# Optimization experiments

Hardware: AMD Instinct MI355X
Metric: run time of the kernel (lower is better)

The kernel has to match this reference:

```python
import jax, jax.numpy as jnp
import numpy as np

B, N, E, L, S = 8, 64, 256, 128, 2  # graphs, nodes, edges, latent dim, MPN steps


def setup_inputs() -> dict:
    key = jax.random.key(0)
    ks = jax.random.split(key, 16)

    def lin(k, fi, fo):
        return (jax.random.normal(k, (fi, fo), jnp.float32) / np.sqrt(fi).astype(np.float32))

    return {
        "x": jax.random.normal(ks[0], (B, N, L), jnp.float32),
        "edge_attr": jax.random.normal(ks[1], (B, E, L), jnp.float32),
        "u": jax.random.normal(ks[2], (B, L), jnp.float32),
        "spdist": jax.random.uniform(ks[3], (B, N, N), jnp.float32),
        "edge_index": jax.random.randint(ks[4], (B, 2, E), 0, N),
        # encoders
        "W_node_enc": lin(ks[5], 2 * L + 1, L), "b_node_enc": jnp.zeros(L, jnp.float32),
        "W_edge_enc": lin(ks[6], L, L), "b_edge_enc": jnp.zeros(L, jnp.float32),
        "W_glob_enc": lin(ks[7], L, L), "b_glob_enc": jnp.zeros(L, jnp.float32),
        # per-step edge / node update MLPs (stacked over S steps)
        "W_edge_upd": jnp.stack([lin(ks[8 + s], 4 * L, L) for s in range(S)]),
        "b_edge_upd": jnp.zeros((S, L), jnp.float32),
        "W_node_upd": jnp.stack([lin(ks[10 + s], 3 * L, L) for s in range(S)]),
        "b_node_upd": jnp.zeros((S, L), jnp.float32),
        # final edge scorer (per_dest_embedding_to_score)
        "W_score": lin(ks[12], L, 1), "b_score": jnp.zeros(1, jnp.float32),
    }


def reference(x, edge_attr, u, spdist, edge_index,
              W_node_enc, b_node_enc, W_edge_enc, b_edge_enc,
              W_glob_enc, b_glob_enc, W_edge_upd, b_edge_upd,
              W_node_upd, b_node_upd, W_score, b_score):
    act = jax.nn.leaky_relu  # torch LeakyReLU default slope 0.01
    n_steps = W_edge_upd.shape[0]

    def per_graph(xg, eg, ug, sdg, eig):
        Ng, Lg = xg.shape
        Eg = eg.shape[0]
        src, dst = eig[0], eig[1]
        # Augmented node features: graph copy d, node i -> [x_i, x_d, spdist[d, i]]
        # (matches x.repeat(N,1) / x.repeat_interleave(N,0) + chunk(N))
        x_tile = jnp.broadcast_to(xg[None, :, :], (Ng, Ng, Lg))
        x_dest = jnp.broadcast_to(xg[:, None, :], (Ng, Ng, Lg))
        xa = jnp.concatenate([x_tile, x_dest, sdg[..., None]], axis=-1)  # [Nd, N, 2L+1]
        h = act(xa @ W_node_enc + b_node_enc)                            # [Nd, N, L]
        ee = act(eg @ W_edge_enc + b_edge_enc)                           # [E, L]
        ee = jnp.broadcast_to(ee[None], (Ng, Eg, Lg))                    # [Nd, E, L]
        gg = act(ug @ W_glob_enc + b_glob_enc)                           # [L]
        for s in range(n_steps):
            gb_e = jnp.broadcast_to(gg, (Ng, Eg, Lg))
            ein = jnp.concatenate([ee, h[:, src], h[:, dst], gb_e], axis=-1)  # [Nd, E, 4L]
            ee = ee + act(ein @ W_edge_upd[s] + b_edge_upd[s])
            agg = jax.vmap(lambda ef: jax.ops.segment_sum(ef, dst, num_segments=Ng))(ee)  # [Nd, N, L]
            gb_n = jnp.broadcast_to(gg, (Ng, Ng, Lg))
            nin = jnp.concatenate([h, agg, gb_n], axis=-1)                    # [Nd, N, 3L]
            h = h + act(nin @ W_node_upd[s] + b_node_upd[s])
        scores = (ee @ W_score + b_score)[..., 0]  # [Nd, E]
        # reshape(N, -1).t().flatten() per graph -> [E * N]
        return scores.T.reshape(-1)

    out = jax.vmap(per_graph)(x, edge_attr, u, spdist, edge_index)  # [B, E*N]
    return out.reshape(-1)
```

## Files before the change

### kernel.cpp

```cpp
#include <hip/hip_runtime.h>
#include <hip/hip_bf16.h>


typedef __attribute__((ext_vector_type(8))) __bf16 bf16x8;
typedef __attribute__((ext_vector_type(4))) __bf16 bf16x4;
typedef __attribute__((ext_vector_type(4))) float  floatx4;

#define MFMA16(a, b, c) __builtin_amdgcn_mfma_f32_16x16x32_bf16((a), (b), (c), 0, 0, 0)

__device__ __forceinline__ float leaky(float x) { return x > 0.f ? x : 0.01f * x; }

#define WS_WT     0
#define WS_XAP    327680
#define WS_XDP    589824
#define WS_EE0    851968
#define WS_CE     1376256
#define WS_CN     1384448
#define WS_CSROFF 1392640
#define WS_CSREID 1394944

#define LDE 140

__global__ __launch_bounds__(256) void mpn_prep(
    const float* __restrict__ x,
    const float* __restrict__ ea,
    const float* __restrict__ u,
    const int*   __restrict__ eidx,
    const float* __restrict__ Wne,
    const float* __restrict__ bne,
    const float* __restrict__ Wee,
    const float* __restrict__ bee,
    const float* __restrict__ Wge,
    const float* __restrict__ bge,
    const float* __restrict__ Weu,
    const float* __restrict__ beu,
    const float* __restrict__ Wnu,
    const float* __restrict__ bnu,
    char* __restrict__ ws)
{
  __shared__ __align__(16) __bf16 smem[384 * LDE];

  const int b = blockIdx.x, tid = threadIdx.x;
  __bf16* wt  = (__bf16*)(ws + WS_WT);
  float*  xap = (float*)(ws + WS_XAP);
  float*  xdp = (float*)(ws + WS_XDP);
  __bf16* ee0 = (__bf16*)(ws + WS_EE0);
  float*  cev = (float*)(ws + WS_CE);
  float*  cnv = (float*)(ws + WS_CN);
  int* csroff = (int*)(ws + WS_CSROFF);
  int* csreid = (int*)(ws + WS_CSREID);

  if (b < 20) {
    const int m = b >> 1, half = b & 1;
    const int s = m / 5, t = m % 5;
    const float* src = (t < 3) ? (Weu + (size_t)(s*512 + t*128)*128)
                               : (Wnu + (size_t)(s*384 + (t-3)*128)*128);
    for (int it = 0; it < 4; ++it) {
      int p = it*256 + tid;
      int mq = half*4 + (p >> 8);
      int c  = (p >> 6) & 3;
      int l  = p & 63;
      int fr = mq*16 + (l & 15);
      int kb = c*32 + (l >> 4)*8;
      __bf16* dst = &wt[m*16384 + ((mq*4 + c)*64 + l)*8];
      #pragma unroll
      for (int j = 0; j < 8; ++j)
        dst[j] = (__bf16)src[(kb + j)*128 + fr];
    }
  } else if (b < 28) {
    const int g = b - 20;
    __shared__ float gg_sh[128];
    __shared__ int dst_sh[256];
    __shared__ int cnt_sh[64];
    __shared__ int off_sh[65];
    if (tid < 128) {
      float acc = bge[tid];
      for (int k = 0; k < 128; ++k)
        acc += u[g*128 + k] * Wge[k*128 + tid];
      gg_sh[tid] = leaky(acc);
    }
    dst_sh[tid] = eidx[g*512 + 256 + tid];
    __syncthreads();
    {
      const int s = tid >> 7, f = tid & 127;
      float ac = beu[s*128 + f];
      float an = bnu[s*128 + f];
      #pragma unroll 8
      for (int k = 0; k < 128; ++k) {
        float gk = gg_sh[k];
        ac += gk * Weu[(s*512 + 384 + k)*128 + f];
        an += gk * Wnu[(s*384 + 256 + k)*128 + f];
      }
      cev[(g*2 + s)*128 + f] = ac;
      cnv[(g*2 + s)*128 + f] = an;
    }
    if (tid < 64) {
      int c = 0;
      for (int e = 0; e < 256; ++e) c += (dst_sh[e] == tid) ? 1 : 0;
      cnt_sh[tid] = c;
    }
    __syncthreads();
    if (tid == 0) {
      int o = 0;
      for (int n = 0; n < 64; ++n) { off_sh[n] = o; o += cnt_sh[n]; }
      off_sh[64] = o;
    }
    __syncthreads();
    if (tid < 65) csroff[g*72 + tid] = off_sh[tid];
    if (tid < 64) {
      int o = off_sh[tid];
      for (int e = 0; e < 256; ++e)
        if (dst_sh[e] == tid) csreid[g*256 + (o++)] = e;
    }
  } else if (b < 36) {
    const int g = b - 28;
    __bf16* s_a = smem;
    __bf16* s_w = smem + 256*LDE;
    #pragma unroll
    for (int it = 0; it < 32; ++it) {
      int c = it*256 + tid;
      int row = c >> 5, f4 = (c & 31)*4;
      floatx4 v = *(const floatx4*)&ea[(size_t)(g*256 + row)*128 + f4];
      bf16x4 o;
      #pragma unroll
      for (int r = 0; r < 4; ++r) o[r] = (__bf16)v[r];
      *(bf16x4*)&s_a[row*LDE + f4] = o;
    }
    #pragma unroll 8
    for (int it = 0; it < 64; ++it) {
      int k = it*2 + (tid >> 7), f = tid & 127;
      s_w[f*LDE + k] = (__bf16)Wee[k*128 + f];
    }
    __syncthreads();
    const int w = tid >> 6, l = tid & 63, q = l >> 4, xn = l & 15;
    bf16x8 bea[4][4];
    #pragma unroll
    for (int t = 0; t < 4; ++t) {
      int e = w*64 + t*16 + xn;
      #pragma unroll
      for (int c = 0; c < 4; ++c)
        bea[t][c] = *(const bf16x8*)&s_a[e*LDE + c*32 + q*8];
    }
    #pragma unroll
    for (int m = 0; m < 8; ++m) {
      floatx4 acc[4];
      #pragma unroll
      for (int t = 0; t < 4; ++t) acc[t] = (floatx4)0.f;
      const int fr = m*16 + xn;
      #pragma unroll
      for (int c = 0; c < 4; ++c) {
        bf16x8 aw = *(const bf16x8*)&s_w[fr*LDE + c*32 + q*8];
        #pragma unroll
        for (int t = 0; t < 4; ++t) acc[t] = MFMA16(aw, bea[t][c], acc[t]);
      }
      const int f0 = m*16 + q*4;
      floatx4 b4 = *(const floatx4*)&bee[f0];
      #pragma unroll
      for (int t = 0; t < 4; ++t) {
        int e = w*64 + t*16 + xn;
        bf16x4 o;
        #pragma unroll
        for (int r = 0; r < 4; ++r) o[r] = (__bf16)leaky(acc[t][r] + b4[r]);
        *(bf16x4*)&ee0[(size_t)(g*256 + e)*128 + f0] = o;
      }
    }
  } else {
    const int g = b - 36;
    __bf16* s_x  = smem;
    __bf16* s_wa = smem + 64*LDE;
    __bf16* s_wb = smem + 192*LDE;
    #pragma unroll
    for (int it = 0; it < 8; ++it) {
      int c = it*256 + tid;
      int row = c >> 5, f4 = (c & 31)*4;
      floatx4 v = *(const floatx4*)&x[(size_t)(g*64 + row)*128 + f4];
      bf16x4 o;
      #pragma unroll
      for (int r = 0; r < 4; ++r) o[r] = (__bf16)v[r];
      *(bf16x4*)&s_x[row*LDE + f4] = o;
    }
    #pragma unroll 8
    for (int it = 0; it < 64; ++it) {
      int k = it*2 + (tid >> 7), f = tid & 127;
      s_wa[f*LDE + k] = (__bf16)Wne[k*128 + f];
      s_wb[f*LDE + k] = (__bf16)Wne[(128 + k)*128 + f];
    }
    __syncthreads();
    const int w = tid >> 6, l = tid & 63, q = l >> 4, xn = l & 15;
    const int i = w*16 + xn;
    bf16x8 bx[4];
    #pragma unroll
    for (int c = 0; c < 4; ++c)
      bx[c] = *(const bf16x8*)&s_x[i*LDE + c*32 + q*8];
    #pragma unroll
    for (int m = 0; m < 8; ++m) {
      floatx4 aa = (floatx4)0.f, ab = (floatx4)0.f;
      const int fr = m*16 + xn;
      #pragma unroll
      for (int c = 0; c < 4; ++c) {
        bf16x8 aw = *(const bf16x8*)&s_wa[fr*LDE + c*32 + q*8];
        aa = MFMA16(aw, bx[c], aa);
      }
      #pragma unroll
      for (int c = 0; c < 4; ++c) {
        bf16x8 aw = *(const bf16x8*)&s_wb[fr*LDE + c*32 + q*8];
        ab = MFMA16(aw, bx[c], ab);
      }
      const int f0 = m*16 + q*4;
      floatx4 bn4 = *(const floatx4*)&bne[f0];
      floatx4 oa;
      #pragma unroll
      for (int r = 0; r < 4; ++r) oa[r] = aa[r] + bn4[r];
      *(floatx4*)&xap[(size_t)(g*64 + i)*128 + f0] = oa;
      *(floatx4*)&xdp[(size_t)(g*64 + i)*128 + f0] = ab;
    }
  }
}

__global__ __launch_bounds__(512, 2) void mpn_main(
    const float* __restrict__ spdist,
    const int*   __restrict__ eidx,
    const float* __restrict__ Wne,
    const float* __restrict__ wscore,
    const float* __restrict__ bscore,
    const char* __restrict__ ws,
    float* __restrict__ out)
{
  __shared__ __align__(16) __bf16 s_ee[256*LDE];
  __shared__ __align__(16) __bf16 s_h [64*LDE];
  __shared__ __align__(16) __bf16 s_p2[64*LDE];
  __shared__ __align__(16) __bf16 s_p3[64*LDE];
  __shared__ int s_off[65];
  __shared__ int s_eid[256];
  __shared__ float s_sc[256];

  const __bf16* wt  = (const __bf16*)(ws + WS_WT);
  const float*  xap = (const float*)(ws + WS_XAP);
  const float*  xdp = (const float*)(ws + WS_XDP);
  const __bf16* ee0 = (const __bf16*)(ws + WS_EE0);
  const float*  cev = (const float*)(ws + WS_CE);
  const float*  cnv = (const float*)(ws + WS_CN);
  const int* csroff = (const int*)(ws + WS_CSROFF);
  const int* csreid = (const int*)(ws + WS_CSREID);

  const int tid = threadIdx.x;
  const int w = tid >> 6, l = tid & 63;
  const int q = l >> 4, xn = l & 15;
  const int wp = w >> 1, mh = w & 1;
  const int lane8 = l*8;
  const int g = blockIdx.x >> 6, d = blockIdx.x & 63;

  if (tid < 65) s_off[tid] = csroff[g*72 + tid];
  if (tid < 256) s_eid[tid] = csreid[g*256 + tid];

  {
    const int f = tid & 127, ib = tid >> 7;
    float xdpv = xdp[(g*64 + d)*128 + f];
    float wspv = Wne[256*128 + f];
    #pragma unroll
    for (int j = 0; j < 16; ++j) {
      int i = ib + 4*j;
      float sp = spdist[(g*64 + d)*64 + i];
      float v = xap[(g*64 + i)*128 + f] + xdpv + sp*wspv;
      s_h[i*LDE + f] = (__bf16)leaky(v);
    }
  }
  #pragma unroll
  for (int it = 0; it < 8; ++it) {
    int c = it*512 + tid;
    int row = c >> 4, col = c & 15;
    *(bf16x8*)&s_ee[row*LDE + col*8] = *(const bf16x8*)&ee0[(g*256 + row)*128 + col*8];
  }

  int mySrc[4], myDst[4];
  #pragma unroll
  for (int t = 0; t < 4; ++t) {
    int e = wp*64 + t*16 + xn;
    mySrc[t] = eidx[g*512 + e];
    myDst[t] = eidx[g*512 + 256 + e];
  }
  __syncthreads();

  for (int s = 0; s < 2; ++s) {
    const __bf16* W1T = wt + (s*5 + 0)*16384;
    const __bf16* W2T = wt + (s*5 + 1)*16384;
    const __bf16* W3T = wt + (s*5 + 2)*16384;
    const __bf16* N1T = wt + (s*5 + 3)*16384;
    const __bf16* N2T = wt + (s*5 + 4)*16384;

    {
      bf16x8 bh[4];
      const int i = wp*16 + xn;
      #pragma unroll
      for (int c = 0; c < 4; ++c)
        bh[c] = *(const bf16x8*)&s_h[i*LDE + c*32 + q*8];
      #pragma unroll
      for (int mm = 0; mm < 4; ++mm) {
        const int m = mh*4 + mm;
        floatx4 a2 = (floatx4)0.f, a3 = (floatx4)0.f;
        #pragma unroll
        for (int c = 0; c < 4; ++c) {
          bf16x8 aw = *(const bf16x8*)&W2T[(m*4 + c)*512 + lane8];
          a2 = MFMA16(aw, bh[c], a2);
        }
        #pragma unroll
        for (int c = 0; c < 4; ++c) {
          bf16x8 aw = *(const bf16x8*)&W3T[(m*4 + c)*512 + lane8];
          a3 = MFMA16(aw, bh[c], a3);
        }
        const int f0 = m*16 + q*4;
        floatx4 ce4 = *(const floatx4*)&cev[(g*2 + s)*128 + f0];
        bf16x4 o2, o3;
        #pragma unroll
        for (int r = 0; r < 4; ++r) { o2[r] = (__bf16)a2[r]; o3[r] = (__bf16)(a3[r] + ce4[r]); }
        *(bf16x4*)&s_p2[i*LDE + f0] = o2;
        *(bf16x4*)&s_p3[i*LDE + f0] = o3;
      }
    }
    __syncthreads();

    {
      bf16x8 be[4][4];
      #pragma unroll
      for (int t = 0; t < 4; ++t) {
        int e = wp*64 + t*16 + xn;
        #pragma unroll
        for (int c = 0; c < 4; ++c)
          be[t][c] = *(const bf16x8*)&s_ee[e*LDE + c*32 + q*8];
      }
      __syncthreads();
      #pragma unroll
      for (int mm = 0; mm < 4; ++mm) {
        const int m = mh*4 + mm;
        floatx4 acc[4];
        #pragma unroll
        for (int t = 0; t < 4; ++t) acc[t] = (floatx4)0.f;
        #pragma unroll
        for (int c = 0; c < 4; ++c) {
          bf16x8 aw = *(const bf16x8*)&W1T[(m*4 + c)*512 + lane8];
          #pragma unroll
          for (int t = 0; t < 4; ++t) acc[t] = MFMA16(aw, be[t][c], acc[t]);
        }
        const int f0 = m*16 + q*4;
        #pragma unroll
        for (int t = 0; t < 4; ++t) {
          int e = wp*64 + t*16 + xn;
          bf16x4 old = *(const bf16x4*)&s_ee[e*LDE + f0];
          bf16x4 v2  = *(const bf16x4*)&s_p2[mySrc[t]*LDE + f0];
          bf16x4 v3  = *(const bf16x4*)&s_p3[myDst[t]*LDE + f0];
          bf16x4 res;
          #pragma unroll
          for (int r = 0; r < 4; ++r) {
            float vv = acc[t][r] + (float)v2[r] + (float)v3[r];
            res[r] = (__bf16)((float)old[r] + leaky(vv));
          }
          *(bf16x4*)&s_ee[e*LDE + f0] = res;
        }
      }
    }
    __syncthreads();

    if (s == 0) {
      {
        const int node = tid >> 3;
        const int fs = (tid & 7)*16;
        float av[16];
        #pragma unroll
        for (int j = 0; j < 16; ++j) av[j] = 0.f;
        const int b0 = s_off[node], b1 = s_off[node + 1];
        for (int idx = b0; idx < b1; ++idx) {
          int e = s_eid[idx];
          #pragma unroll
          for (int cc = 0; cc < 2; ++cc) {
            bf16x8 vv = *(const bf16x8*)&s_ee[e*LDE + fs + cc*8];
            #pragma unroll
            for (int j = 0; j < 8; ++j) av[cc*8 + j] += (float)vv[j];
          }
        }
        #pragma unroll
        for (int cc = 0; cc < 2; ++cc) {
          bf16x8 o;
          #pragma unroll
          for (int j = 0; j < 8; ++j) o[j] = (__bf16)av[cc*8 + j];
          *(bf16x8*)&s_p2[node*LDE + fs + cc*8] = o;
        }
      }
      __syncthreads();
      {
        bf16x8 bh[4], bg[4];
        const int i = wp*16 + xn;
        #pragma unroll
        for (int c = 0; c < 4; ++c) {
          bh[c] = *(const bf16x8*)&s_h[i*LDE + c*32 + q*8];
          bg[c] = *(const bf16x8*)&s_p2[i*LDE + c*32 + q*8];
        }
        __syncthreads();
        #pragma unroll
        for (int mm = 0; mm < 4; ++mm) {
          const int m = mh*4 + mm;
          floatx4 acc = (floatx4)0.f;
          #pragma unroll
          for (int c = 0; c < 4; ++c) {
            bf16x8 aw = *(const bf16x8*)&N1T[(m*4 + c)*512 + lane8];
            acc = MFMA16(aw, bh[c], acc);
          }
          #pragma unroll
          for (int c = 0; c < 4; ++c) {
            bf16x8 aw = *(const bf16x8*)&N2T[(m*4 + c)*512 + lane8];
            acc = MFMA16(aw, bg[c], acc);
          }
          const int f0 = m*16 + q*4;
          floatx4 cn4 = *(const floatx4*)&cnv[(g*2 + s)*128 + f0];
          bf16x4 old = *(const bf16x4*)&s_h[i*LDE + f0];
          bf16x4 res;
          #pragma unroll
          for (int r = 0; r < 4; ++r)
            res[r] = (__bf16)((float)old[r] + leaky(acc[r] + cn4[r]));
          *(bf16x4*)&s_h[i*LDE + f0] = res;
        }
      }
      __syncthreads();
    }
  }

  {
    const int e = tid & 255, hh = tid >> 8;
    float acc = 0.f;
    #pragma unroll
    for (int c = 0; c < 8; ++c) {
      bf16x8 vv = *(const bf16x8*)&s_ee[e*LDE + hh*64 + c*8];
      #pragma unroll
      for (int j = 0; j < 8; ++j) acc += (float)vv[j] * wscore[hh*64 + c*8 + j];
    }
    if (hh == 1) s_sc[e] = acc;
    __syncthreads();
    if (hh == 0) out[g*16384 + e*64 + d] = acc + s_sc[e] + bscore[0];
  }
}

extern "C" void kernel_launch(void* const* d_in, const int* in_sizes, int n_in,
                              void* d_out, int out_size, void* d_ws, size_t ws_size,
                              hipStream_t stream) {
  (void)in_sizes; (void)n_in; (void)out_size; (void)ws_size;
  const float* x   = (const float*)d_in[0];
  const float* ea  = (const float*)d_in[1];
  const float* u   = (const float*)d_in[2];
  const float* sp  = (const float*)d_in[3];
  const int*   ei  = (const int*)d_in[4];
  const float* Wne = (const float*)d_in[5];
  const float* bne = (const float*)d_in[6];
  const float* Wee = (const float*)d_in[7];
  const float* bee = (const float*)d_in[8];
  const float* Wge = (const float*)d_in[9];
  const float* bge = (const float*)d_in[10];
  const float* Weu = (const float*)d_in[11];
  const float* beu = (const float*)d_in[12];
  const float* Wnu = (const float*)d_in[13];
  const float* bnu = (const float*)d_in[14];
  const float* Wsc = (const float*)d_in[15];
  const float* bsc = (const float*)d_in[16];
  char* ws = (char*)d_ws;

  hipLaunchKernelGGL(mpn_prep, dim3(44), dim3(256), 0, stream,
                     x, ea, u, ei, Wne, bne, Wee, bee, Wge, bge, Weu, beu, Wnu, bnu, ws);
  hipLaunchKernelGGL(mpn_main, dim3(512), dim3(512), 0, stream,
                     sp, ei, Wne, Wsc, bsc, (const char*)ws, (float*)d_out);
}
```

Before: 160.0 us.

## Repartition MFMA work so each wave owns output features and keeps weights in registers

Each wave now owns a fixed 16-column slice of output features instead of a (row group, feature half) split. It loads its weight fragments from global memory once into registers and streams node or edge rows from LDS across all rows. This removes repeated global weight loads per output tile in favour of more LDS reads of activations. It also raises register pressure, since the kernel now holds 16 accumulators and 16 src/dst indices per lane.

```diff
diff --git a/kernel.cpp b/kernel.cpp
--- a/kernel.cpp
+++ b/kernel.cpp
@@ -246,8 +246,8 @@
   const int tid = threadIdx.x;
   const int w = tid >> 6, l = tid & 63;
   const int q = l >> 4, xn = l & 15;
-  const int wp = w >> 1, mh = w & 1;
   const int lane8 = l*8;
+  const int fme = w*16 + q*4;
   const int g = blockIdx.x >> 6, d = blockIdx.x & 63;
 
   if (tid < 65) s_off[tid] = csroff[g*72 + tid];
@@ -272,10 +272,10 @@
     *(bf16x8*)&s_ee[row*LDE + col*8] = *(const bf16x8*)&ee0[(g*256 + row)*128 + col*8];
   }
 
-  int mySrc[4], myDst[4];
+  int mySrc[16], myDst[16];
   #pragma unroll
-  for (int t = 0; t < 4; ++t) {
-    int e = wp*64 + t*16 + xn;
+  for (int t = 0; t < 16; ++t) {
+    int e = t*16 + xn;
     mySrc[t] = eidx[g*512 + e];
     myDst[t] = eidx[g*512 + 256 + e];
   }
@@ -289,73 +289,63 @@
     const __bf16* N2T = wt + (s*5 + 4)*16384;
 
     {
-      bf16x8 bh[4];
-      const int i = wp*16 + xn;
+      bf16x8 aw2[4], aw3[4];
+      #pragma unroll
+      for (int c = 0; c < 4; ++c) {
+        aw2[c] = *(const bf16x8*)&W2T[(w*4 + c)*512 + lane8];
+        aw3[c] = *(const bf16x8*)&W3T[(w*4 + c)*512 + lane8];
+      }
+      floatx4 ce4 = *(const floatx4*)&cev[(g*2 + s)*128 + fme];
+      #pragma unroll
+      for (int t = 0; t < 4; ++t) {
+        const int i = t*16 + xn;
+        floatx4 a2 = (floatx4)0.f, a3 = (floatx4)0.f;
+        #pragma unroll
+        for (int c = 0; c < 4; ++c) {
+          bf16x8 bh = *(const bf16x8*)&s_h[i*LDE + c*32 + q*8];
+          a2 = MFMA16(aw2[c], bh, a2);
+          a3 = MFMA16(aw3[c], bh, a3);
+        }
+        bf16x4 o2, o3;
+        #pragma unroll
+        for (int r = 0; r < 4; ++r) { o2[r] = (__bf16)a2[r]; o3[r] = (__bf16)(a3[r] + ce4[r]); }
+        *(bf16x4*)&s_p2[i*LDE + fme] = o2;
+        *(bf16x4*)&s_p3[i*LDE + fme] = o3;
+      }
+    }
+    __syncthreads();
+
+    {
+      bf16x8 aw1[4];
       #pragma unroll
       for (int c = 0; c < 4; ++c)
-        bh[c] = *(const bf16x8*)&s_h[i*LDE + c*32 + q*8];
-      #pragma unroll
-      for (int mm = 0; mm < 4; ++mm) {
-        const int m = mh*4 + mm;
-        floatx4 a2 = (floatx4)0.f, a3 = (floatx4)0.f;
+        aw1[c] = *(const bf16x8*)&W1T[(w*4 + c)*512 + lane8];
+      floatx4 acc[16];
+      #pragma unroll
+      for (int t = 0; t < 16; ++t) {
+        const int e = t*16 + xn;
+        floatx4 a = (floatx4)0.f;
         #pragma unroll
         for (int c = 0; c < 4; ++c) {
-          bf16x8 aw = *(const bf16x8*)&W2T[(m*4 + c)*512 + lane8];
-          a2 = MFMA16(aw, bh[c], a2);
-        }
-        #pragma unroll
-        for (int c = 0; c < 4; ++c) {
-          bf16x8 aw = *(const bf16x8*)&W3T[(m*4 + c)*512 + lane8];
-          a3 = MFMA16(aw, bh[c], a3);
-        }
-        const int f0 = m*16 + q*4;
-        floatx4 ce4 = *(const floatx4*)&cev[(g*2 + s)*128 + f0];
-        bf16x4 o2, o3;
-        #pragma unroll
-        for (int r = 0; r < 4; ++r) { o2[r] = (__bf16)a2[r]; o3[r] = (__bf16)(a3[r] + ce4[r]); }
-        *(bf16x4*)&s_p2[i*LDE + f0] = o2;
-        *(bf16x4*)&s_p3[i*LDE + f0] = o3;
-      }
-    }
-    __syncthreads();
-
-    {
-      bf16x8 be[4][4];
-      #pragma unroll
-      for (int t = 0; t < 4; ++t) {
-        int e = wp*64 + t*16 + xn;
-        #pragma unroll
-        for (int c = 0; c < 4; ++c)
-          be[t][c] = *(const bf16x8*)&s_ee[e*LDE + c*32 + q*8];
+          bf16x8 be = *(const bf16x8*)&s_ee[e*LDE + c*32 + q*8];
+          a = MFMA16(aw1[c], be, a);
+        }
+        acc[t] = a;
       }
       __syncthreads();
       #pragma unroll
-      for (int mm = 0; mm < 4; ++mm) {
-        const int m = mh*4 + mm;
-        floatx4 acc[4];
-        #pragma unroll
-        for (int t = 0; t < 4; ++t) acc[t] = (floatx4)0.f;
-        #pragma unroll
-        for (int c = 0; c < 4; ++c) {
-          bf16x8 aw = *(const bf16x8*)&W1T[(m*4 + c)*512 + lane8];
-          #pragma unroll
-          for (int t = 0; t < 4; ++t) acc[t] = MFMA16(aw, be[t][c], acc[t]);
-        }
-        const int f0 = m*16 + q*4;
-        #pragma unroll
-        for (int t = 0; t < 4; ++t) {
-          int e = wp*64 + t*16 + xn;
-          bf16x4 old = *(const bf16x4*)&s_ee[e*LDE + f0];
-          bf16x4 v2  = *(const bf16x4*)&s_p2[mySrc[t]*LDE + f0];
-          bf16x4 v3  = *(const bf16x4*)&s_p3[myDst[t]*LDE + f0];
-          bf16x4 res;
-          #pragma unroll
-          for (int r = 0; r < 4; ++r) {
-            float vv = acc[t][r] + (float)v2[r] + (float)v3[r];
-            res[r] = (__bf16)((float)old[r] + leaky(vv));
-          }
-          *(bf16x4*)&s_ee[e*LDE + f0] = res;
-        }
+      for (int t = 0; t < 16; ++t) {
+        const int e = t*16 + xn;
+        bf16x4 old = *(const bf16x4*)&s_ee[e*LDE + fme];
+        bf16x4 v2  = *(const bf16x4*)&s_p2[mySrc[t]*LDE + fme];
+        bf16x4 v3  = *(const bf16x4*)&s_p3[myDst[t]*LDE + fme];
+        bf16x4 res;
+        #pragma unroll
+        for (int r = 0; r < 4; ++r) {
+          float vv = acc[t][r] + (float)v2[r] + (float)v3[r];
+          res[r] = (__bf16)((float)old[r] + leaky(vv));
+        }
+        *(bf16x4*)&s_ee[e*LDE + fme] = res;
       }
     }
     __syncthreads();
@@ -387,36 +377,40 @@
       }
       __syncthreads();
       {
-        bf16x8 bh[4], bg[4];
-        const int i = wp*16 + xn;
+        bf16x8 an1[4], an2[4];
         #pragma unroll
         for (int c = 0; c < 4; ++c) {
-          bh[c] = *(const bf16x8*)&s_h[i*LDE + c*32 + q*8];
-          bg[c] = *(const bf16x8*)&s_p2[i*LDE + c*32 + q*8];
-        }
-        __syncthreads();
-        #pragma unroll
-        for (int mm = 0; mm < 4; ++mm) {
-          const int m = mh*4 + mm;
-          floatx4 acc = (floatx4)0.f;
+          an1[c] = *(const bf16x8*)&N1T[(w*4 + c)*512 + lane8];
+          an2[c] = *(const bf16x8*)&N2T[(w*4 + c)*512 + lane8];
+        }
+        floatx4 acc4[4];
+        #pragma unroll
+        for (int t = 0; t < 4; ++t) {
+          const int i = t*16 + xn;
+          floatx4 a = (floatx4)0.f;
           #pragma unroll
           for (int c = 0; c < 4; ++c) {
-            bf16x8 aw = *(const bf16x8*)&N1T[(m*4 + c)*512 + lane8];
-            acc = MFMA16(aw, bh[c], acc);
+            bf16x8 bh = *(const bf16x8*)&s_h[i*LDE + c*32 + q*8];
+            a = MFMA16(an1[c], bh, a);
           }
           #pragma unroll
           for (int c = 0; c < 4; ++c) {
-            bf16x8 aw = *(const bf16x8*)&N2T[(m*4 + c)*512 + lane8];
-            acc = MFMA16(aw, bg[c], acc);
+            bf16x8 bg = *(const bf16x8*)&s_p2[i*LDE + c*32 + q*8];
+            a = MFMA16(an2[c], bg, a);
           }
-          const int f0 = m*16 + q*4;
-          floatx4 cn4 = *(const floatx4*)&cnv[(g*2 + s)*128 + f0];
-          bf16x4 old = *(const bf16x4*)&s_h[i*LDE + f0];
+          acc4[t] = a;
+        }
+        __syncthreads();
+        floatx4 cn4 = *(const floatx4*)&cnv[(g*2 + s)*128 + fme];
+        #pragma unroll
+        for (int t = 0; t < 4; ++t) {
+          const int i = t*16 + xn;
+          bf16x4 old = *(const bf16x4*)&s_h[i*LDE + fme];
           bf16x4 res;
           #pragma unroll
           for (int r = 0; r < 4; ++r)
-            res[r] = (__bf16)((float)old[r] + leaky(acc[r] + cn4[r]));
-          *(bf16x4*)&s_h[i*LDE + f0] = res;
+            res[r] = (__bf16)((float)old[r] + leaky(acc4[t][r] + cn4[r]));
+          *(bf16x4*)&s_h[i*LDE + fme] = res;
         }
       }
       __syncthreads();
```

Result: no change. 158.3 us (-1.1%).

## Double main kernel block to 1024 threads and remap edge/node MFMA work

Applied to the files above, without the earlier changes.

The main kernel now launches 1024 threads per block, with each wave owning 16 edges for the edge update instead of 64, and node-side matmuls split across twice as many waves. Since LDS use (~108KB) caps occupancy at one block per CU, this doubles the waves available to hide MFMA and LDS latency. Each wave touches only its own edge rows, which lets one barrier in the edge update be removed. The scoring reduction is also split four ways. The launch bound of (1024,4) may force a tight register budget and risks spills, since acc[8] is now held across the whole edge update.

```diff
diff --git a/kernel.cpp b/kernel.cpp
--- a/kernel.cpp
+++ b/kernel.cpp
@@ -217,7 +217,7 @@
   }
 }
 
-__global__ __launch_bounds__(512, 2) void mpn_main(
+__global__ __launch_bounds__(1024, 4) void mpn_main(
     const float* __restrict__ spdist,
     const int*   __restrict__ eidx,
     const float* __restrict__ Wne,
@@ -232,7 +232,7 @@
   __shared__ __align__(16) __bf16 s_p3[64*LDE];
   __shared__ int s_off[65];
   __shared__ int s_eid[256];
-  __shared__ float s_sc[256];
+  __shared__ float s_scf[1024];
 
   const __bf16* wt  = (const __bf16*)(ws + WS_WT);
   const float*  xap = (const float*)(ws + WS_XAP);
@@ -246,9 +246,10 @@
   const int tid = threadIdx.x;
   const int w = tid >> 6, l = tid & 63;
   const int q = l >> 4, xn = l & 15;
-  const int wp = w >> 1, mh = w & 1;
+  const int tw = w & 3, mp = w >> 2;
   const int lane8 = l*8;
   const int g = blockIdx.x >> 6, d = blockIdx.x & 63;
+  const int myE = w*16 + xn;
 
   if (tid < 65) s_off[tid] = csroff[g*72 + tid];
   if (tid < 256) s_eid[tid] = csreid[g*256 + tid];
@@ -258,27 +259,22 @@
     float xdpv = xdp[(g*64 + d)*128 + f];
     float wspv = Wne[256*128 + f];
     #pragma unroll
-    for (int j = 0; j < 16; ++j) {
-      int i = ib + 4*j;
+    for (int j = 0; j < 8; ++j) {
+      int i = ib + 8*j;
       float sp = spdist[(g*64 + d)*64 + i];
       float v = xap[(g*64 + i)*128 + f] + xdpv + sp*wspv;
       s_h[i*LDE + f] = (__bf16)leaky(v);
     }
   }
   #pragma unroll
-  for (int it = 0; it < 8; ++it) {
-    int c = it*512 + tid;
+  for (int it = 0; it < 4; ++it) {
+    int c = it*1024 + tid;
     int row = c >> 4, col = c & 15;
     *(bf16x8*)&s_ee[row*LDE + col*8] = *(const bf16x8*)&ee0[(g*256 + row)*128 + col*8];
   }
 
-  int mySrc[4], myDst[4];
-  #pragma unroll
-  for (int t = 0; t < 4; ++t) {
-    int e = wp*64 + t*16 + xn;
-    mySrc[t] = eidx[g*512 + e];
-    myDst[t] = eidx[g*512 + 256 + e];
-  }
+  const int se = eidx[g*512 + myE];
+  const int de = eidx[g*512 + 256 + myE];
   __syncthreads();
 
   for (int s = 0; s < 2; ++s) {
@@ -290,13 +286,13 @@
 
     {
       bf16x8 bh[4];
-      const int i = wp*16 + xn;
+      const int i = tw*16 + xn;
       #pragma unroll
       for (int c = 0; c < 4; ++c)
         bh[c] = *(const bf16x8*)&s_h[i*LDE + c*32 + q*8];
       #pragma unroll
-      for (int mm = 0; mm < 4; ++mm) {
-        const int m = mh*4 + mm;
+      for (int mm = 0; mm < 2; ++mm) {
+        const int m = mp*2 + mm;
         floatx4 a2 = (floatx4)0.f, a3 = (floatx4)0.f;
         #pragma unroll
         for (int c = 0; c < 4; ++c) {
@@ -320,102 +316,94 @@
     __syncthreads();
 
     {
-      bf16x8 be[4][4];
-      #pragma unroll
-      for (int t = 0; t < 4; ++t) {
-        int e = wp*64 + t*16 + xn;
-        #pragma unroll
-        for (int c = 0; c < 4; ++c)
-          be[t][c] = *(const bf16x8*)&s_ee[e*LDE + c*32 + q*8];
-      }
-      __syncthreads();
-      #pragma unroll
-      for (int mm = 0; mm < 4; ++mm) {
-        const int m = mh*4 + mm;
-        floatx4 acc[4];
-        #pragma unroll
-        for (int t = 0; t < 4; ++t) acc[t] = (floatx4)0.f;
+      bf16x8 be[4];
+      #pragma unroll
+      for (int c = 0; c < 4; ++c)
+        be[c] = *(const bf16x8*)&s_ee[myE*LDE + c*32 + q*8];
+      floatx4 acc[8];
+      #pragma unroll
+      for (int m = 0; m < 8; ++m) {
+        floatx4 a = (floatx4)0.f;
         #pragma unroll
         for (int c = 0; c < 4; ++c) {
           bf16x8 aw = *(const bf16x8*)&W1T[(m*4 + c)*512 + lane8];
-          #pragma unroll
-          for (int t = 0; t < 4; ++t) acc[t] = MFMA16(aw, be[t][c], acc[t]);
-        }
+          a = MFMA16(aw, be[c], a);
+        }
+        acc[m] = a;
+      }
+      #pragma unroll
+      for (int m = 0; m < 8; ++m) {
         const int f0 = m*16 + q*4;
-        #pragma unroll
-        for (int t = 0; t < 4; ++t) {
-          int e = wp*64 + t*16 + xn;
-          bf16x4 old = *(const bf16x4*)&s_ee[e*LDE + f0];
-          bf16x4 v2  = *(const bf16x4*)&s_p2[mySrc[t]*LDE + f0];
-          bf16x4 v3  = *(const bf16x4*)&s_p3[myDst[t]*LDE + f0];
-          bf16x4 res;
-          #pragma unroll
-          for (int r = 0; r < 4; ++r) {
-            float vv = acc[t][r] + (float)v2[r] + (float)v3[r];
-            res[r] = (__bf16)((float)old[r] + leaky(vv));
-          }
-          *(bf16x4*)&s_ee[e*LDE + f0] = res;
-        }
+        bf16x4 old = *(const bf16x4*)&s_ee[myE*LDE + f0];
+        bf16x4 v2  = *(const bf16x4*)&s_p2[se*LDE + f0];
+        bf16x4 v3  = *(const bf16x4*)&s_p3[de*LDE + f0];
+        bf16x4 res;
+        #pragma unroll
+        for (int r = 0; r < 4; ++r) {
+          float vv = acc[m][r] + (float)v2[r] + (float)v3[r];
+          res[r] = (__bf16)((float)old[r] + leaky(vv));
+        }
+        *(bf16x4*)&s_ee[myE*LDE + f0] = res;
       }
     }
     __syncthreads();
 
     if (s == 0) {
       {
-        const int node = tid >> 3;
-        const int fs = (tid & 7)*16;
-        float av[16];
-        #pragma unroll
-        for (int j = 0; j < 16; ++j) av[j] = 0.f;
+        const int node = tid >> 4;
+        const int fs = (tid & 15)*8;
+        float av[8];
+        #pragma unroll
+        for (int j = 0; j < 8; ++j) av[j] = 0.f;
         const int b0 = s_off[node], b1 = s_off[node + 1];
         for (int idx = b0; idx < b1; ++idx) {
           int e = s_eid[idx];
+          bf16x8 vv = *(const bf16x8*)&s_ee[e*LDE + fs];
           #pragma unroll
-          for (int cc = 0; cc < 2; ++cc) {
-            bf16x8 vv = *(const bf16x8*)&s_ee[e*LDE + fs + cc*8];
-            #pragma unroll
-            for (int j = 0; j < 8; ++j) av[cc*8 + j] += (float)vv[j];
-          }
-        }
-        #pragma unroll
-        for (int cc = 0; cc < 2; ++cc) {
-          bf16x8 o;
-          #pragma unroll
-          for (int j = 0; j < 8; ++j) o[j] = (__bf16)av[cc*8 + j];
-          *(bf16x8*)&s_p2[node*LDE + fs + cc*8] = o;
-        }
+          for (int j = 0; j < 8; ++j) av[j] += (float)vv[j];
+        }
+        bf16x8 o;
+        #pragma unroll
+        for (int j = 0; j < 8; ++j) o[j] = (__bf16)av[j];
+        *(bf16x8*)&s_p2[node*LDE + fs] = o;
       }
       __syncthreads();
       {
         bf16x8 bh[4], bg[4];
-        const int i = wp*16 + xn;
+        const int i = tw*16 + xn;
         #pragma unroll
         for (int c = 0; c < 4; ++c) {
           bh[c] = *(const bf16x8*)&s_h[i*LDE + c*32 + q*8];
           bg[c] = *(const bf16x8*)&s_p2[i*LDE + c*32 + q*8];
         }
-        __syncthreads();
-        #pragma unroll
-        for (int mm = 0; mm < 4; ++mm) {
-          const int m = mh*4 + mm;
-          floatx4 acc = (floatx4)0.f;
+        floatx4 acc2[2];
+        #pragma unroll
+        for (int mm = 0; mm < 2; ++mm) {
+          const int m = mp*2 + mm;
+          floatx4 a = (floatx4)0.f;
           #pragma unroll
           for (int c = 0; c < 4; ++c) {
             bf16x8 aw = *(const bf16x8*)&N1T[(m*4 + c)*512 + lane8];
-            acc = MFMA16(aw, bh[c], acc);
+            a = MFMA16(aw, bh[c], a);
           }
           #pragma unroll
           for (int c = 0; c < 4; ++c) {
             bf16x8 aw = *(const bf16x8*)&N2T[(m*4 + c)*512 + lane8];
-            acc = MFMA16(aw, bg[c], acc);
+            a = MFMA16(aw, bg[c], a);
           }
+          acc2[mm] = a;
+        }
+        __syncthreads();
+        #pragma unroll
+        for (int mm = 0; mm < 2; ++mm) {
+          const int m = mp*2 + mm;
           const int f0 = m*16 + q*4;
           floatx4 cn4 = *(const floatx4*)&cnv[(g*2 + s)*128 + f0];
           bf16x4 old = *(const bf16x4*)&s_h[i*LDE + f0];
           bf16x4 res;
           #pragma unroll
           for (int r = 0; r < 4; ++r)
-            res[r] = (__bf16)((float)old[r] + leaky(acc[r] + cn4[r]));
+            res[r] = (__bf16)((float)old[r] + leaky(acc2[mm][r] + cn4[r]));
           *(bf16x4*)&s_h[i*LDE + f0] = res;
         }
       }
@@ -424,17 +412,19 @@
   }
 
   {
-    const int e = tid & 255, hh = tid >> 8;
+    const int e = tid >> 2, part = tid & 3;
+    const int ks = part*32;
     float acc = 0.f;
     #pragma unroll
-    for (int c = 0; c < 8; ++c) {
-      bf16x8 vv = *(const bf16x8*)&s_ee[e*LDE + hh*64 + c*8];
-      #pragma unroll
-      for (int j = 0; j < 8; ++j) acc += (float)vv[j] * wscore[hh*64 + c*8 + j];
-    }
-    if (hh == 1) s_sc[e] = acc;
-    __syncthreads();
-    if (hh == 0) out[g*16384 + e*64 + d] = acc + s_sc[e] + bscore[0];
+    for (int c = 0; c < 4; ++c) {
+      bf16x8 vv = *(const bf16x8*)&s_ee[e*LDE + ks + c*8];
+      #pragma unroll
+      for (int j = 0; j < 8; ++j) acc += (float)vv[j] * wscore[ks + c*8 + j];
+    }
+    s_scf[tid] = acc;
+    __syncthreads();
+    if (part == 0)
+      out[g*16384 + e*64 + d] = s_scf[tid] + s_scf[tid+1] + s_scf[tid+2] + s_scf[tid+3] + bscore[0];
   }
 }
 
@@ -463,6 +453,6 @@
 
   hipLaunchKernelGGL(mpn_prep, dim3(44), dim3(256), 0, stream,
                      x, ea, u, ei, Wne, bne, Wee, bee, Wge, bge, Weu, beu, Wnu, bnu, ws);
-  hipLaunchKernelGGL(mpn_main, dim3(512), dim3(512), 0, stream,
+  hipLaunchKernelGGL(mpn_main, dim3(512), dim3(1024), 0, stream,
                      sp, ei, Wne, Wsc, bsc, (const char*)ws, (float*)d_out);
 }
```

Result: slower. 169.7 us (+6.0%).
